# Kernel tuning notes

Measured on AMD Instinct MI355X. Metric: run time of the kernel, lower is better.

## Reference

```python
import jax, jax.numpy as jnp
import numpy as np

B, T, N, DIN, HID, ED, K = 64, 12, 1024, 2, 64, 10, 2

def setup_inputs() -> dict:
    key = jax.random.key(0)
    ks = jax.random.split(key, 18)
    g = lambda i, shape, s=0.1: jax.random.normal(ks[i], shape, jnp.float32) * s
    return dict(
        x=g(0, (B, T, N, DIN), 1.0),
        node_embeddings=g(1, (N, ED), 1.0),
        # GCRN cell 0 (dim_in=DIN): gate -> 2*HID, update -> HID
        Wg0=g(2, (ED, K, DIN + HID, 2 * HID)), bg0=g(3, (ED, 2 * HID)),
        Wu0=g(4, (ED, K, DIN + HID, HID)),     bu0=g(5, (ED, HID)),
        # GCRN cell 1 (dim_in=HID)
        Wg1=g(6, (ED, K, 2 * HID, 2 * HID)),   bg1=g(7, (ED, 2 * HID)),
        Wu1=g(8, (ED, K, 2 * HID, HID)),       bu1=g(9, (ED, HID)),
        # RelatinoShipConv: pointwise Linear(input_dim -> rnn_units), torch [out,in]
        Wr=g(10, (HID, DIN)), br=g(11, (HID,)),
        # end_conv1: Linear(HID,HID, bias=False) (num_layers>1 branch)
        W1=g(12, (HID, HID)),
        # self.conv: Conv2d(horizon, horizon, (1, HID+1), bias=False), OIHW
        Wc=g(13, (T, T, 1, HID + 1)),
        # end_conv2: Conv2d(horizon, horizon, (1, HID), bias)
        W2=g(14, (T, T, 1, HID)), b2=g(15, (T,)),
        # end_conv3: Conv2d(horizon, horizon, (1, 2), dilation (1, HID), bias)
        W3=g(16, (T, T, 1, 2)), b3=g(17, (T,)),
    )

def _avwgcn(x, supports, E, Wp, bp):
    # x:[B,N,C], supports:[K,N,N], E:[N,ED] -> [B,N,O]  (AGCRN adaptive graph conv)
    xg = jnp.einsum('knm,bmc->bnkc', supports, x)
    W = jnp.einsum('ne,ekio->nkio', E, Wp)
    b = E @ bp
    return jnp.einsum('bnki,nkio->bno', xg, W) + b

def _cell(xt, h, supports, E, Wg, bg, Wu, bu):
    # GCRN GRU cell
    zr = jax.nn.sigmoid(_avwgcn(jnp.concatenate([xt, h], -1), supports, E, Wg, bg))
    z, r = jnp.split(zr, 2, -1)
    hc = jnp.tanh(_avwgcn(jnp.concatenate([xt, z * h], -1), supports, E, Wu, bu))
    return r * h + (1.0 - r) * hc

def _conv2d(x, w, b=None, rhs_dilation=(1, 1)):
    y = jax.lax.conv_general_dilated(x, w, (1, 1), 'VALID',
        rhs_dilation=rhs_dilation, dimension_numbers=('NCHW', 'OIHW', 'NCHW'))
    return y if b is None else y + b[None, :, None, None]

def _forward(x, E, Wg0, bg0, Wu0, bu0, Wg1, bg1, Wu1, bu1, Wr, br, W1, Wc, W2, b2, W3, b3):
    A = jax.nn.softmax(jax.nn.relu(E @ E.T), axis=1)
    supports = jnp.stack([jnp.eye(N, dtype=x.dtype), A], 0)  # [K,N,N]
    # GCRN encoder: python loop over 2 layers, lax.scan over the 12 timesteps
    cur = x
    for (Wg, bg, Wu, bu) in ((Wg0, bg0, Wu0, bu0), (Wg1, bg1, Wu1, bu1)):
        h0 = jnp.zeros((x.shape[0], N, HID), x.dtype)
        def step(h, xt):
            h = _cell(xt, h, supports, E, Wg, bg, Wu, bu)
            return h, h
        _, hs = jax.lax.scan(step, h0, jnp.swapaxes(cur, 0, 1))
        cur = jnp.swapaxes(hs, 0, 1)  # [B,T,N,HID]
    out = cur @ W1.T  # end_conv1 (Linear, no bias); dropout is identity in eval
    relation = x @ Wr.T + br  # [B,T,N,HID]
    # torch einsum 'btnc,knn->kbcnt' takes the DIAGONAL of supports over n
    rg = jnp.einsum('btnc,knn->kbcnt', relation, supports)
    rg = jnp.transpose(rg, (1, 4, 3, 2, 0)).reshape(x.shape[0], T, N, -1)  # [B,12,N,2*HID]
    rst = _conv2d(rg, Wc)  # [B,12,N,HID]
    out = _conv2d(jnp.concatenate([rst, out], -1), W2, b2)  # [B,12,N,HID+1]
    out = _conv2d(out, W3, b3, rhs_dilation=(1, HID))       # [B,12,N,1]
    return out

def reference(x, node_embeddings, Wg0, bg0, Wu0, bu0, Wg1, bg1, Wu1, bu1, Wr, br, W1, Wc, W2, b2, W3, b3):
    return _forward(x, node_embeddings, Wg0, bg0, Wu0, bu0, Wg1, bg1, Wu1, bu1, Wr, br, W1, Wc, W2, b2, W3, b3)
```

## Files before the change

kernel.cpp:

```cpp
#include <hip/hip_runtime.h>

typedef unsigned short u16;
typedef unsigned int   u32;


__device__ __forceinline__ float bf2f(u16 u){ return __uint_as_float(((u32)u)<<16); }
__device__ __forceinline__ u16 f2bf(float f){
  u32 u = __float_as_uint(f);
  return (u16)((u + 0x7fffu + ((u>>16)&1u)) >> 16);
}

__global__ __launch_bounds__(256) void k_A2(const float* __restrict__ E,
    float* __restrict__ At, float* __restrict__ diagA)
{
  __shared__ float EL[10][1024];
  __shared__ float row[1024];
  __shared__ float red[4];
  int n = blockIdx.x, tid = threadIdx.x;
  for (int idx=tid; idx<10240; idx+=256)
    EL[idx>>10][idx&1023] = E[(idx&1023)*10 + (idx>>10)];
  __syncthreads();
  float en[10];
#pragma unroll
  for (int e=0;e<10;++e) en[e] = EL[e][n];
  float lmax = -1e30f;
#pragma unroll
  for (int j=0;j<4;++j){
    int m = tid*4 + j;
    float d = 0.f;
#pragma unroll
    for (int e=0;e<10;++e) d = fmaf(en[e], EL[e][m], d);
    d = fmaxf(d, 0.f);
    row[m] = d; lmax = fmaxf(lmax, d);
  }
#pragma unroll
  for (int o=32;o>0;o>>=1) lmax = fmaxf(lmax, __shfl_xor(lmax, o));
  if ((tid&63)==0) red[tid>>6] = lmax;
  __syncthreads();
  float mx = fmaxf(fmaxf(red[0],red[1]), fmaxf(red[2],red[3]));
  __syncthreads();
  float lsum = 0.f;
#pragma unroll
  for (int j=0;j<4;++j){
    int m = tid*4 + j;
    float ex = expf(row[m] - mx);
    row[m] = ex; lsum += ex;
  }
#pragma unroll
  for (int o=32;o>0;o>>=1) lsum += __shfl_xor(lsum, o);
  if ((tid&63)==0) red[tid>>6] = lsum;
  __syncthreads();
  float inv = 1.f/(red[0]+red[1]+red[2]+red[3]);
#pragma unroll
  for (int j=0;j<4;++j){
    int m = tid*4 + j;
    float v = row[m]*inv;
    At[(size_t)m*1024 + n] = v;
    if (m == n) diagA[n] = v;
  }
}

__global__ __launch_bounds__(64) void k_b3eff(
    const float* __restrict__ b2, const float* __restrict__ W3,
    const float* __restrict__ b3, float* __restrict__ b3eff)
{
  int o = threadIdx.x;
  if (o < 12){
    float a = b3[o];
    for (int i=0;i<12;++i)
      a += b2[i] * (W3[(o*12+i)*2] + W3[(o*12+i)*2+1]);
    b3eff[o] = a;
  }
}

__global__ __launch_bounds__(256) void k_Vpre(const float* __restrict__ W1,
    const float* __restrict__ W2, float* __restrict__ V)
{
  int idx = blockIdx.x*256 + threadIdx.x;
  if (idx >= 9216) return;
  int c = idx & 63, r = idx >> 6;
  int j = r % 12, i = r / 12;
  float a = 0.f;
  for (int o=0;o<64;++o)
    a = fmaf(W2[(i*12+j)*64+o], W1[o*64+c], a);
  V[idx] = a;
}

__global__ __launch_bounds__(256) void k_Gpre(const float* __restrict__ Wc,
    const float* __restrict__ W2, u16* __restrict__ G)
{
  int idx = blockIdx.x*256 + threadIdx.x;
  int u = idx & 127, r = idx >> 7;
  int ip = r % 12, i = r / 12;
  float a = 0.f;
  int wlo = u>64 ? u-64 : 0;
  int whi = u<63 ? u : 63;
  for (int j=0;j<12;++j){
    const float* w2r = W2 + (i*12+j)*64;
    const float* wcr = Wc + (j*12+ip)*65;
    for (int w=wlo; w<=whi; ++w)
      a = fmaf(w2r[w], wcr[u-w], a);
  }
  G[idx] = f2bf(a);
}

__global__ __launch_bounds__(256) void k_combF(const float* __restrict__ Wp,
    const float* __restrict__ E, float* __restrict__ out, int plane)
{
  int n = blockIdx.x;
  int j = blockIdx.y*256 + threadIdx.x;
  if (j >= plane) return;
  float a = 0.f;
#pragma unroll
  for (int e=0;e<10;++e) a = fmaf(E[n*10+e], Wp[(size_t)e*plane + j], a);
  out[(size_t)n*plane + j] = a;
}

__global__ __launch_bounds__(256) void gemm9(const float* __restrict__ At,
    const float* __restrict__ X0, float* __restrict__ Y0,
    const float* __restrict__ X1, float* __restrict__ Y1)
{
  int flat = blockIdx.x + (blockIdx.y<<3) + (blockIdx.z<<8);
  int xt = flat & 7;
  int ys = (flat>>3) & 31;
  int zs = flat >> 8;
  const float* X = zs ? X1 : X0;
  float*       Y = zs ? Y1 : Y0;
  int n0 = xt * 128;
  long baseA = (long)(2*ys) * 65536;
  long baseB = baseA + 65536;
  __shared__ float Al[2][16*128];
  __shared__ float Xl[2][16*128];
  int tid = threadIdx.x;
  int tx = tid & 15, ty = tid >> 4;
  int ka = tid >> 5,  na = (tid & 31)*4;
  int cx = tid & 31;
  long xoff = (cx < 16) ? (baseA + (long)cx*4) : (baseB + (long)(cx-16)*4);

  float accA[8][4], accB[8][4];
#pragma unroll
  for (int r=0;r<8;++r)
#pragma unroll
    for (int c=0;c<4;++c){ accA[r][c]=0.f; accB[r][c]=0.f; }

  float4 ra0 = *(const float4*)(At + (size_t)ka*1024 + n0 + na);
  float4 ra1 = *(const float4*)(At + (size_t)(ka+8)*1024 + n0 + na);
  float4 rx0 = *(const float4*)(X + xoff + (long)ka*64);
  float4 rx1 = *(const float4*)(X + xoff + (long)(ka+8)*64);

  for (int m0=0; m0<1024; m0+=16){
    int cur = (m0>>4)&1;
    *(float4*)(Al[cur] + tid*4)       = ra0;
    *(float4*)(Al[cur] + (tid+256)*4) = ra1;
    *(float4*)(Xl[cur] + tid*4)       = rx0;
    *(float4*)(Xl[cur] + (tid+256)*4) = rx1;
    __syncthreads();
    if (m0+16 < 1024){
      int m1 = m0+16;
      ra0 = *(const float4*)(At + (size_t)(m1+ka)*1024 + n0 + na);
      ra1 = *(const float4*)(At + (size_t)(m1+ka+8)*1024 + n0 + na);
      rx0 = *(const float4*)(X + xoff + (long)(m1+ka)*64);
      rx1 = *(const float4*)(X + xoff + (long)(m1+ka+8)*64);
    }
#pragma unroll
    for (int kk=0;kk<16;++kk){
      float4 a0 = *(const float4*)(Al[cur] + kk*128 + ty*4);
      float4 a1 = *(const float4*)(Al[cur] + kk*128 + 64 + ty*4);
      float4 x0 = *(const float4*)(Xl[cur] + kk*128 + tx*4);
      float4 x1 = *(const float4*)(Xl[cur] + kk*128 + 64 + tx*4);
      float av[8] = {a0.x,a0.y,a0.z,a0.w,a1.x,a1.y,a1.z,a1.w};
      float xa[4] = {x0.x,x0.y,x0.z,x0.w};
      float xb[4] = {x1.x,x1.y,x1.z,x1.w};
#pragma unroll
      for (int r=0;r<8;++r)
#pragma unroll
        for (int c=0;c<4;++c){
          accA[r][c] = fmaf(av[r], xa[c], accA[r][c]);
          accB[r][c] = fmaf(av[r], xb[c], accB[r][c]);
        }
    }
  }
#pragma unroll
  for (int r=0;r<8;++r){
    int row = n0 + (r>>2)*64 + ty*4 + (r&3);
    float4 vA; vA.x=accA[r][0]; vA.y=accA[r][1]; vA.z=accA[r][2]; vA.w=accA[r][3];
    float4 vB; vB.x=accB[r][0]; vB.y=accB[r][1]; vB.z=accB[r][2]; vB.w=accB[r][3];
    *(float4*)&Y[baseA + (long)row*64 + tx*4] = vA;
    *(float4*)&Y[baseB + (long)row*64 + tx*4] = vB;
  }
}

__global__ __launch_bounds__(256) void gemm2x(const float* __restrict__ At,
    const float* __restrict__ x, float* __restrict__ Y)
{
  __shared__ float Ats[64][65];
  __shared__ float Xs[64][65];
  int n0 = blockIdx.x*64;
  int q0 = blockIdx.y*64;
  int tid = threadIdx.x, c = tid & 63, rq = tid >> 6;
  float acc[16];
#pragma unroll
  for (int j=0;j<16;++j) acc[j]=0.f;
  for (int m0=0; m0<1024; m0+=64){
#pragma unroll
    for (int j=0;j<16;++j){
      int idx = tid + j*256;
      int k = idx>>6, r = idx&63;
      Ats[k][r] = At[(size_t)(m0+k)*1024 + n0 + r];
      int qg = q0 + r;
      Xs[k][r] = x[(size_t)(qg>>1)*2048 + (size_t)(m0+k)*2 + (qg&1)];
    }
    __syncthreads();
    for (int k=0;k<64;++k){
      float xv = Xs[k][c];
#pragma unroll
      for (int j=0;j<16;++j) acc[j] = fmaf(Ats[k][rq+4*j], xv, acc[j]);
    }
    __syncthreads();
  }
#pragma unroll
  for (int j=0;j<16;++j)
    Y[(size_t)(n0+rq+4*j)*1536 + q0 + c] = acc[j];
}

template<int L>
__device__ __forceinline__ void gate_body(
    float* __restrict__ inp, float* __restrict__ Wl, float* __restrict__ En,
    const float* __restrict__ Wg, const float* __restrict__ Wpre,
    const float* __restrict__ bgp, const float* __restrict__ E,
    const float* __restrict__ xsrc, const float* __restrict__ Axt,
    const float* __restrict__ h, const float* __restrict__ Ah,
    float* __restrict__ zh, float* __restrict__ rb, int t, int first,
    int n, int b0, int tid)
{
  constexpr int IX  = (L==0)?2:64;
  constexpr int KI  = 2*(IX+64);
  constexpr int CH  = (L==0)?44:32;
  constexpr int NCH = KI/CH;
  constexpr int O   = 128;

  if (tid < 10) En[tid] = E[n*10 + tid];
  for (int idx=tid; idx<32*IX; idx+=256){
    int bl = idx/IX, i = idx - bl*IX; int b = b0+bl;
    inp[bl*KI + i] = (L==0)
      ? xsrc[(size_t)((b*12+t)*1024+n)*2 + i]
      : xsrc[((size_t)b<<16) + (size_t)n*64 + i];
  }
  for (int idx=tid; idx<2048; idx+=256){
    int bl = idx>>6, c = idx&63; int b = b0+bl;
    inp[bl*KI + IX + c] = first ? 0.f : h[((size_t)b<<16) + (size_t)n*64 + c];
  }
  for (int idx=tid; idx<32*IX; idx+=256){
    int bl = idx/IX, i = idx - bl*IX; int b = b0+bl;
    inp[bl*KI + IX+64+i] = (L==0)
      ? Axt[(size_t)n*1536 + (size_t)(b*12+t)*2 + i]
      : Axt[((size_t)b<<16) + (size_t)n*64 + i];
  }
  for (int idx=tid; idx<2048; idx+=256){
    int bl = idx>>6, c = idx&63; int b = b0+bl;
    inp[bl*KI + 2*IX+64+c] = first ? 0.f : Ah[((size_t)b<<16) + (size_t)n*64 + c];
  }
  __syncthreads();

  int bg = tid >> 5;
  int og = tid & 31;
  float acc[4][4];
#pragma unroll
  for (int d=0;d<4;++d){
    int o = og*4+d;
    float a = 0.f;
#pragma unroll
    for (int e=0;e<10;++e) a = fmaf(En[e], bgp[e*O+o], a);
#pragma unroll
    for (int bl=0;bl<4;++bl) acc[bl][d] = a;
  }

  for (int ch=0; ch<NCH; ++ch){
    if (Wpre){
      const float* src = Wpre + (size_t)n*(KI*O) + ch*CH*O;
      for (int idx=tid; idx<CH*O; idx+=256) Wl[idx] = src[idx];
    } else {
      for (int idx=tid; idx<CH*O; idx+=256){
        int i = idx>>7, o = idx&127;
        float a = 0.f;
#pragma unroll
        for (int e=0;e<10;++e)
          a = fmaf(En[e], Wg[((size_t)e*KI + ch*CH + i)*O + o], a);
        Wl[i*O + o] = a;
      }
    }
    __syncthreads();
    float4 xq[4], wq[4];
#pragma unroll
    for (int bl=0;bl<4;++bl) xq[bl] = *(const float4*)&inp[(bg*4+bl)*KI + ch*CH];
#pragma unroll
    for (int ii=0;ii<4;++ii) wq[ii] = *(const float4*)&Wl[ii*O + og*4];
    for (int i=0; i<CH; i+=4){
      int i2 = (i+4<CH) ? i+4 : i;
      float4 xq2[4], wq2[4];
#pragma unroll
      for (int bl=0;bl<4;++bl) xq2[bl] = *(const float4*)&inp[(bg*4+bl)*KI + ch*CH + i2];
#pragma unroll
      for (int ii=0;ii<4;++ii) wq2[ii] = *(const float4*)&Wl[(i2+ii)*O + og*4];
      float xv[4][4], wv[4][4];
#pragma unroll
      for (int bl=0;bl<4;++bl){ xv[bl][0]=xq[bl].x; xv[bl][1]=xq[bl].y; xv[bl][2]=xq[bl].z; xv[bl][3]=xq[bl].w; }
#pragma unroll
      for (int ii=0;ii<4;++ii){ wv[ii][0]=wq[ii].x; wv[ii][1]=wq[ii].y; wv[ii][2]=wq[ii].z; wv[ii][3]=wq[ii].w; }
#pragma unroll
      for (int bl=0;bl<4;++bl)
#pragma unroll
        for (int d=0;d<4;++d)
#pragma unroll
          for (int ii=0;ii<4;++ii)
            acc[bl][d] = fmaf(xv[bl][ii], wv[ii][d], acc[bl][d]);
#pragma unroll
      for (int bl=0;bl<4;++bl) xq[bl]=xq2[bl];
#pragma unroll
      for (int ii=0;ii<4;++ii) wq[ii]=wq2[ii];
    }
    __syncthreads();
  }

#pragma unroll
  for (int bl=0;bl<4;++bl){
    int b = b0 + bg*4 + bl;
    size_t base = ((size_t)b<<16) + (size_t)n*64;
#pragma unroll
    for (int d=0;d<4;++d){
      int o = og*4 + d;
      float s = 1.f/(1.f+__expf(-acc[bl][d]));
      if (o < 64){
        if (!first) zh[base+o] = s * h[base+o];
      } else {
        rb[base+o-64] = s;
      }
    }
  }
}

__global__ __launch_bounds__(256) void k_gateB(int l_z0,
    const float* __restrict__ Wg0, const float* __restrict__ Wg0p,
    const float* __restrict__ bg0,
    const float* __restrict__ Wg1, const float* __restrict__ Wg1p,
    const float* __restrict__ bg1,
    const float* __restrict__ E,  const float* __restrict__ x,
    const float* __restrict__ Ax0T,
    const float* __restrict__ h0cur, const float* __restrict__ h1,
    const float* __restrict__ Axt1,  const float* __restrict__ AhZ1,
    float* __restrict__ zh0, float* __restrict__ rb0,
    float* __restrict__ zh1, float* __restrict__ rb1,
    int t0, int first0, int first1)
{
  __shared__ float smem[12288];
  __shared__ float En[10];
  int n = blockIdx.x, b0 = blockIdx.y*32, tid = threadIdx.x;
  int L = blockIdx.z ? 0 : l_z0;
  if (L == 1)
    gate_body<1>(smem, smem + 32*256, En, Wg1, Wg1p, bg1, E,
                 h0cur, Axt1, h1, AhZ1, zh1, rb1, 0, first1, n, b0, tid);
  else
    gate_body<0>(smem, smem + 32*132, En, Wg0, Wg0p, bg0, E,
                 x, Ax0T, h0cur, Axt1, zh0, rb0, t0, first0, n, b0, tid);
}

template<int L>
__device__ __forceinline__ void upd_body(
    float* __restrict__ inp, float* __restrict__ Wl, float* __restrict__ En,
    const float* __restrict__ Wu, const float* __restrict__ Wpre,
    const float* __restrict__ bup, const float* __restrict__ E,
    const float* __restrict__ xsrc, const float* __restrict__ Axt,
    const float* __restrict__ zh, const float* __restrict__ Azh,
    const float* __restrict__ rb,
    const float* __restrict__ hread, float* __restrict__ hwrite,
    const float* __restrict__ V, float* __restrict__ q1acc,
    int t, int tq, int first, int n, int b0, int tid)
{
  constexpr int IX  = (L==0)?2:64;
  constexpr int KI  = 2*(IX+64);
  constexpr int CH  = (L==0)?44:64;
  constexpr int NCH = KI/CH;
  constexpr int O   = 64;

  if (tid < 10) En[tid] = E[n*10 + tid];
  for (int idx=tid; idx<32*IX; idx+=256){
    int bl = idx/IX, i = idx - bl*IX; int b = b0+bl;
    inp[bl*KI + i] = (L==0)
      ? xsrc[(size_t)((b*12+t)*1024+n)*2 + i]
      : xsrc[((size_t)b<<16) + (size_t)n*64 + i];
  }
  for (int idx=tid; idx<2048; idx+=256){
    int bl = idx>>6, c = idx&63; int b = b0+bl;
    inp[bl*KI + IX + c] = first ? 0.f : zh[((size_t)b<<16) + (size_t)n*64 + c];
  }
  for (int idx=tid; idx<32*IX; idx+=256){
    int bl = idx/IX, i = idx - bl*IX; int b = b0+bl;
    inp[bl*KI + IX+64+i] = (L==0)
      ? Axt[(size_t)n*1536 + (size_t)(b*12+t)*2 + i]
      : Axt[((size_t)b<<16) + (size_t)n*64 + i];
  }
  for (int idx=tid; idx<2048; idx+=256){
    int bl = idx>>6, c = idx&63; int b = b0+bl;
    inp[bl*KI + 2*IX+64+c] = first ? 0.f : Azh[((size_t)b<<16) + (size_t)n*64 + c];
  }
  __syncthreads();

  int bg = tid >> 5;
  int og = tid & 31;
  float acc[4][2];
#pragma unroll
  for (int d=0;d<2;++d){
    int o = og*2+d;
    float a = 0.f;
#pragma unroll
    for (int e=0;e<10;++e) a = fmaf(En[e], bup[e*O+o], a);
#pragma unroll
    for (int bl=0;bl<4;++bl) acc[bl][d] = a;
  }

  for (int ch=0; ch<NCH; ++ch){
    if (Wpre){
      const float* src = Wpre + (size_t)n*(KI*O) + ch*CH*O;
      for (int idx=tid; idx<CH*O; idx+=256) Wl[idx] = src[idx];
    } else {
      for (int idx=tid; idx<CH*O; idx+=256){
        int i = idx>>6, o = idx&63;
        float a = 0.f;
#pragma unroll
        for (int e=0;e<10;++e)
          a = fmaf(En[e], Wu[((size_t)e*KI + ch*CH + i)*O + o], a);
        Wl[i*O + o] = a;
      }
    }
    __syncthreads();
    float4 xq[4]; float2 wq[4];
#pragma unroll
    for (int bl=0;bl<4;++bl) xq[bl] = *(const float4*)&inp[(bg*4+bl)*KI + ch*CH];
#pragma unroll
    for (int ii=0;ii<4;++ii) wq[ii] = *(const float2*)&Wl[ii*O + og*2];
    for (int i=0; i<CH; i+=4){
      int i2 = (i+4<CH) ? i+4 : i;
      float4 xq2[4]; float2 wq2[4];
#pragma unroll
      for (int bl=0;bl<4;++bl) xq2[bl] = *(const float4*)&inp[(bg*4+bl)*KI + ch*CH + i2];
#pragma unroll
      for (int ii=0;ii<4;++ii) wq2[ii] = *(const float2*)&Wl[(i2+ii)*O + og*2];
      float xv[4][4], wv[4][2];
#pragma unroll
      for (int bl=0;bl<4;++bl){ xv[bl][0]=xq[bl].x; xv[bl][1]=xq[bl].y; xv[bl][2]=xq[bl].z; xv[bl][3]=xq[bl].w; }
#pragma unroll
      for (int ii=0;ii<4;++ii){ wv[ii][0]=wq[ii].x; wv[ii][1]=wq[ii].y; }
#pragma unroll
      for (int bl=0;bl<4;++bl)
#pragma unroll
        for (int d=0;d<2;++d)
#pragma unroll
          for (int ii=0;ii<4;++ii)
            acc[bl][d] = fmaf(xv[bl][ii], wv[ii][d], acc[bl][d]);
#pragma unroll
      for (int bl=0;bl<4;++bl) xq[bl]=xq2[bl];
#pragma unroll
      for (int ii=0;ii<4;++ii) wq[ii]=wq2[ii];
    }
    __syncthreads();
  }

  float* hnL = Wl;
  float* VL  = Wl + 2080;
#pragma unroll
  for (int bl=0;bl<4;++bl){
    int b = b0 + bg*4 + bl;
    size_t base = ((size_t)b<<16) + (size_t)n*64;
#pragma unroll
    for (int d=0;d<2;++d){
      int o = og*2 + d;
      float hc = tanhf(acc[bl][d]);
      float r  = rb[base+o];
      float h0v = first ? 0.f : hread[base+o];
      float hn = r*h0v + (1.f-r)*hc;
      hwrite[base+o] = hn;
      if (L==1) hnL[(bg*4+bl)*65 + o] = hn;
    }
  }
  if (L==1){
    for (int idx=tid; idx<768; idx+=256)
      VL[idx] = V[((idx>>6)*12+tq)*64 + (idx&63)];
    __syncthreads();
    for (int task=tid; task<384; task+=256){
      int bl = task & 31, i = task >> 5;
      const float* hv = hnL + bl*65;
      const float* vv = VL + i*64;
      float s = 0.f;
#pragma unroll 8
      for (int c=0;c<64;++c) s = fmaf(hv[c], vv[c], s);
      size_t qi = (((size_t)(b0+bl)<<10) + n)*12 + i;
      if (first) q1acc[qi] = s; else q1acc[qi] += s;
    }
  }
}

__global__ __launch_bounds__(256) void k_updB(int l_z0,
    const float* __restrict__ Wu0, const float* __restrict__ Wu0p,
    const float* __restrict__ bu0,
    const float* __restrict__ Wu1, const float* __restrict__ Wu1p,
    const float* __restrict__ bu1,
    const float* __restrict__ E,  const float* __restrict__ x,
    const float* __restrict__ Ax0T, const float* __restrict__ Axt1,
    const float* __restrict__ h0cur, float* __restrict__ h0new,
    float* __restrict__ h1,
    const float* __restrict__ zh0, const float* __restrict__ Azh0,
    const float* __restrict__ rb0,
    const float* __restrict__ zh1, const float* __restrict__ Azh1,
    const float* __restrict__ rb1,
    const float* __restrict__ V, float* __restrict__ q1acc,
    int t0, int t1, int first0, int first1)
{
  __shared__ float smem[12288];
  __shared__ float En[10];
  int n = blockIdx.x, b0 = blockIdx.y*32, tid = threadIdx.x;
  int L = blockIdx.z ? 0 : l_z0;
  if (L == 1)
    upd_body<1>(smem, smem + 32*256, En, Wu1, Wu1p, bu1, E,
                h0cur, Axt1, zh1, Azh1, rb1, h1, h1, V, q1acc,
                0, t1, first1, n, b0, tid);
  else
    upd_body<0>(smem, smem + 32*132, En, Wu0, Wu0p, bu0, E,
                x, Ax0T, zh0, Azh0, rb0, h0cur, h0new, nullptr, nullptr,
                t0, 0, first0, n, b0, tid);
}

__global__ __launch_bounds__(256) void k_q0G(
    const float* __restrict__ x, const float* __restrict__ diagA,
    const u16* __restrict__ G,
    const float* __restrict__ Wr, const float* __restrict__ br,
    float* __restrict__ q0buf)
{
  int n = blockIdx.x, tid = threadIdx.x;
  __shared__ u16  GL[18432];
  __shared__ float xsL[64][25];
  __shared__ float WrL[64][2];
  __shared__ float brL[64];

  for (int idx=tid; idx<18432; idx+=256) GL[idx] = G[idx];
  for (int idx=tid; idx<1536; idx+=256){
    int b = idx/24, r = idx - b*24;
    xsL[b][r] = x[(size_t)((b*12+(r>>1))*1024+n)*2 + (r&1)];
  }
  if (tid<128) WrL[tid>>1][tid&1] = Wr[tid];
  else if (tid<192) brL[tid-128] = br[tid-128];
  __syncthreads();

  float dA = diagA[n];
  int b = tid & 63, iq = tid >> 6;
  int i0 = iq*3;
  float q0a=0.f, q0b=0.f, q0c=0.f;
  for (int ip=0; ip<12; ++ip){
    float xa = xsL[b][ip*2], xb = xsL[b][ip*2+1];
    const u16* g0r = &GL[((i0+0)*12+ip)*128];
    const u16* g1r = &GL[((i0+1)*12+ip)*128];
    const u16* g2r = &GL[((i0+2)*12+ip)*128];
    for (int c=0;c<64;++c){
      float rel  = fmaf(xa, WrL[c][0], fmaf(xb, WrL[c][1], brL[c]));
      float relD = rel * dA;
      u32 g0 = *(const u32*)&g0r[2*c];
      u32 g1 = *(const u32*)&g1r[2*c];
      u32 g2 = *(const u32*)&g2r[2*c];
      q0a = fmaf(rel, bf2f((u16)g0), fmaf(relD, bf2f((u16)(g0>>16)), q0a));
      q0b = fmaf(rel, bf2f((u16)g1), fmaf(relD, bf2f((u16)(g1>>16)), q0b));
      q0c = fmaf(rel, bf2f((u16)g2), fmaf(relD, bf2f((u16)(g2>>16)), q0c));
    }
  }
  size_t qb = (((size_t)b<<10) + n)*12;
  q0buf[qb+i0]   = q0a;
  q0buf[qb+i0+1] = q0b;
  q0buf[qb+i0+2] = q0c;
}

__global__ __launch_bounds__(256) void k_head2(
    const float* __restrict__ q0buf, const float* __restrict__ q1acc,
    const float* __restrict__ W3, const float* __restrict__ b3eff,
    float* __restrict__ out)
{
  int n = blockIdx.x, tid = threadIdx.x;
  __shared__ float W3L[12][12][2];
  __shared__ float b3eL[12];
  __shared__ float q0L[64][12];
  __shared__ float q1L[64][12];

  if (tid < 12) b3eL[tid] = b3eff[tid];
  for (int idx=tid; idx<288; idx+=256){
    int o = idx/24, r = idx - o*24;
    W3L[o][r>>1][r&1] = W3[idx];
  }
  for (int idx=tid; idx<768; idx+=256){
    int b = idx/12, i = idx - (idx/12)*12;
    size_t base = (((size_t)b<<10) + n)*12 + i;
    q0L[b][i] = q0buf[base];
    q1L[b][i] = q1acc[base];
  }
  __syncthreads();

  for (int idx=tid; idx<768; idx+=256){
    int bb = idx/12, o = idx - (idx/12)*12;
    float a = b3eL[o];
#pragma unroll
    for (int i=0;i<12;++i)
      a += q0L[bb][i]*W3L[o][i][0] + q1L[bb][i]*W3L[o][i][1];
    out[(size_t)(bb*12+o)*1024 + n] = a;
  }
}

extern "C" void kernel_launch(void* const* d_in, const int* in_sizes, int n_in,
                              void* d_out, int out_size, void* d_ws, size_t ws_size,
                              hipStream_t stream)
{
  const float* x   = (const float*)d_in[0];
  const float* E   = (const float*)d_in[1];
  const float* Wg0 = (const float*)d_in[2];
  const float* bg0 = (const float*)d_in[3];
  const float* Wu0 = (const float*)d_in[4];
  const float* bu0 = (const float*)d_in[5];
  const float* Wg1 = (const float*)d_in[6];
  const float* bg1 = (const float*)d_in[7];
  const float* Wu1 = (const float*)d_in[8];
  const float* bu1 = (const float*)d_in[9];
  const float* Wr  = (const float*)d_in[10];
  const float* br  = (const float*)d_in[11];
  const float* W1  = (const float*)d_in[12];
  const float* Wc  = (const float*)d_in[13];
  const float* W2  = (const float*)d_in[14];
  const float* b2  = (const float*)d_in[15];
  const float* W3  = (const float*)d_in[16];
  const float* b3  = (const float*)d_in[17];

  char* ws = (char*)d_ws;
  size_t off = 0;
  auto alloc = [&](size_t bytes)->void*{
    void* p = ws + off; off += (bytes + 255) & ~(size_t)255; return p;
  };
  float* At    = (float*)alloc(1024ull*1024*4);
  float* diagA = (float*)alloc(1024*4);
  float* Ax0T  = (float*)alloc(1024ull*1536*4);
  float* Axt1  = (float*)alloc(64ull*65536*4);
  float* AhZ1  = (float*)alloc(64ull*65536*4);
  float* Azh0  = (float*)alloc(64ull*65536*4);
  float* Azh1  = (float*)alloc(64ull*65536*4);
  float* zh0   = (float*)alloc(64ull*65536*4);
  float* zh1   = (float*)alloc(64ull*65536*4);
  float* rb0   = (float*)alloc(64ull*65536*4);
  float* rb1   = (float*)alloc(64ull*65536*4);
  float* h0a   = (float*)alloc(64ull*65536*4);
  float* h0b   = (float*)alloc(64ull*65536*4);
  float* h1    = (float*)alloc(64ull*65536*4);
  float* q1acc = (float*)alloc(64ull*1024*12*4);
  float* q0buf = (float*)alloc(64ull*1024*12*4);
  float* V     = (float*)alloc(12ull*12*64*4);
  u16*   G     = (u16*)alloc(12ull*12*128*2);
  float* b3eff = (float*)alloc(12*4);

  if (off > ws_size) return;

  auto tryAlloc = [&](size_t bytes)->float*{
    size_t aligned = (bytes + 255) & ~(size_t)255;
    if (off + aligned > ws_size) return (float*)nullptr;
    void* p = ws + off; off += aligned; return (float*)p;
  };
  float* Wg1c = tryAlloc(1024ull*32768*4);
  float* Wu1c = tryAlloc(1024ull*16384*4);
  float* Wg0c = tryAlloc(1024ull*16896*4);
  float* Wu0c = tryAlloc(1024ull*8448*4);

  k_A2<<<dim3(1024),256,0,stream>>>(E, At, diagA);
  k_b3eff<<<dim3(1),64,0,stream>>>(b2, W3, b3, b3eff);
  k_Vpre<<<dim3(36),256,0,stream>>>(W1, W2, V);
  k_Gpre<<<dim3(72),256,0,stream>>>(Wc, W2, G);
  if (Wg1c) k_combF<<<dim3(1024,128),256,0,stream>>>(Wg1, E, Wg1c, 32768);
  if (Wu1c) k_combF<<<dim3(1024, 64),256,0,stream>>>(Wu1, E, Wu1c, 16384);
  if (Wg0c) k_combF<<<dim3(1024, 66),256,0,stream>>>(Wg0, E, Wg0c, 16896);
  if (Wu0c) k_combF<<<dim3(1024, 33),256,0,stream>>>(Wu0, E, Wu0c,  8448);
  gemm2x<<<dim3(16,24),256,0,stream>>>(At, x, Ax0T);
  k_q0G<<<dim3(1024),256,0,stream>>>(x, diagA, G, Wr, br, q0buf);

  k_gateB<<<dim3(1024,2,1),256,0,stream>>>(0, Wg0,Wg0c,bg0, Wg1,Wg1c,bg1,
      E, x, Ax0T, h0a, h1, Axt1, AhZ1, zh0, rb0, zh1, rb1, 0, 1, 0);
  k_updB<<<dim3(1024,2,1),256,0,stream>>>(0, Wu0,Wu0c,bu0, Wu1,Wu1c,bu1,
      E, x, Ax0T, Axt1, h0a, h0a, h1, zh0, Azh0, rb0, zh1, Azh1, rb1,
      V, q1acc, 0, 0, 1, 0);
  gemm9<<<dim3(8,32,1),256,0,stream>>>(At, h0a, Axt1, nullptr, nullptr);

  for (int k=0; k<12; ++k){
    int last   = (k == 11);
    int first1 = (k == 0);
    float* h0cur = (k&1) ? h0b : h0a;
    float* h0new = (k&1) ? h0a : h0b;

    k_gateB<<<dim3(1024,2, last?1:2),256,0,stream>>>(1, Wg0,Wg0c,bg0,
        Wg1,Wg1c,bg1, E, x, Ax0T, h0cur, h1, Axt1, AhZ1,
        zh0, rb0, zh1, rb1, k+1, 0, first1);

    if (first1)
      gemm9<<<dim3(8,32,1),256,0,stream>>>(At, zh0, Azh0, nullptr, nullptr);
    else if (last)
      gemm9<<<dim3(8,32,1),256,0,stream>>>(At, zh1, Azh1, nullptr, nullptr);
    else
      gemm9<<<dim3(8,32,2),256,0,stream>>>(At, zh1, Azh1, zh0, Azh0);

    k_updB<<<dim3(1024,2, last?1:2),256,0,stream>>>(1, Wu0,Wu0c,bu0,
        Wu1,Wu1c,bu1, E, x, Ax0T, Axt1, h0cur, h0new, h1,
        zh0, Azh0, rb0, zh1, Azh1, rb1, V, q1acc, k+1, k, 0, first1);

    if (!last)
      gemm9<<<dim3(8,32,2),256,0,stream>>>(At, h1, AhZ1, h0new, Axt1);
  }

  k_head2<<<dim3(1024),256,0,stream>>>(q0buf, q1acc, W3, b3eff, (float*)d_out);
}
```

Baseline: 9.957 ms.

## Process all 64 batches per node block to halve per-node weight loads

```diff
diff --git a/kernel.cpp b/kernel.cpp
--- a/kernel.cpp
+++ b/kernel.cpp
@@ -225,54 +225,53 @@
 
 template<int L>
 __device__ __forceinline__ void gate_body(
-    float* __restrict__ inp, float* __restrict__ Wl, float* __restrict__ En,
+    float* __restrict__ inp, float* __restrict__ Wl,
     const float* __restrict__ Wg, const float* __restrict__ Wpre,
     const float* __restrict__ bgp, const float* __restrict__ E,
     const float* __restrict__ xsrc, const float* __restrict__ Axt,
     const float* __restrict__ h, const float* __restrict__ Ah,
     float* __restrict__ zh, float* __restrict__ rb, int t, int first,
-    int n, int b0, int tid)
+    int n, int tid)
 {
   constexpr int IX  = (L==0)?2:64;
   constexpr int KI  = 2*(IX+64);
-  constexpr int CH  = (L==0)?44:32;
+  constexpr int CH  = (L==0)?44:16;
   constexpr int NCH = KI/CH;
   constexpr int O   = 128;
 
-  if (tid < 10) En[tid] = E[n*10 + tid];
-  for (int idx=tid; idx<32*IX; idx+=256){
-    int bl = idx/IX, i = idx - bl*IX; int b = b0+bl;
+  for (int idx=tid; idx<64*IX; idx+=256){
+    int bl = idx/IX, i = idx - bl*IX;
     inp[bl*KI + i] = (L==0)
-      ? xsrc[(size_t)((b*12+t)*1024+n)*2 + i]
-      : xsrc[((size_t)b<<16) + (size_t)n*64 + i];
-  }
-  for (int idx=tid; idx<2048; idx+=256){
-    int bl = idx>>6, c = idx&63; int b = b0+bl;
-    inp[bl*KI + IX + c] = first ? 0.f : h[((size_t)b<<16) + (size_t)n*64 + c];
-  }
-  for (int idx=tid; idx<32*IX; idx+=256){
-    int bl = idx/IX, i = idx - bl*IX; int b = b0+bl;
+      ? xsrc[(size_t)((bl*12+t)*1024+n)*2 + i]
+      : xsrc[((size_t)bl<<16) + (size_t)n*64 + i];
+  }
+  for (int idx=tid; idx<4096; idx+=256){
+    int bl = idx>>6, c = idx&63;
+    inp[bl*KI + IX + c] = first ? 0.f : h[((size_t)bl<<16) + (size_t)n*64 + c];
+  }
+  for (int idx=tid; idx<64*IX; idx+=256){
+    int bl = idx/IX, i = idx - bl*IX;
     inp[bl*KI + IX+64+i] = (L==0)
-      ? Axt[(size_t)n*1536 + (size_t)(b*12+t)*2 + i]
-      : Axt[((size_t)b<<16) + (size_t)n*64 + i];
-  }
-  for (int idx=tid; idx<2048; idx+=256){
-    int bl = idx>>6, c = idx&63; int b = b0+bl;
-    inp[bl*KI + 2*IX+64+c] = first ? 0.f : Ah[((size_t)b<<16) + (size_t)n*64 + c];
+      ? Axt[(size_t)n*1536 + (size_t)(bl*12+t)*2 + i]
+      : Axt[((size_t)bl<<16) + (size_t)n*64 + i];
+  }
+  for (int idx=tid; idx<4096; idx+=256){
+    int bl = idx>>6, c = idx&63;
+    inp[bl*KI + 2*IX+64+c] = first ? 0.f : Ah[((size_t)bl<<16) + (size_t)n*64 + c];
   }
   __syncthreads();
 
   int bg = tid >> 5;
   int og = tid & 31;
-  float acc[4][4];
+  float acc[8][4];
 #pragma unroll
   for (int d=0;d<4;++d){
     int o = og*4+d;
     float a = 0.f;
 #pragma unroll
-    for (int e=0;e<10;++e) a = fmaf(En[e], bgp[e*O+o], a);
-#pragma unroll
-    for (int bl=0;bl<4;++bl) acc[bl][d] = a;
+    for (int e=0;e<10;++e) a = fmaf(E[n*10+e], bgp[e*O+o], a);
+#pragma unroll
+    for (int bb=0;bb<8;++bb) acc[bb][d] = a;
   }
 
   for (int ch=0; ch<NCH; ++ch){
@@ -285,51 +284,41 @@
         float a = 0.f;
 #pragma unroll
         for (int e=0;e<10;++e)
-          a = fmaf(En[e], Wg[((size_t)e*KI + ch*CH + i)*O + o], a);
+          a = fmaf(E[n*10+e], Wg[((size_t)e*KI + ch*CH + i)*O + o], a);
         Wl[i*O + o] = a;
       }
     }
     __syncthreads();
-    float4 xq[4], wq[4];
-#pragma unroll
-    for (int bl=0;bl<4;++bl) xq[bl] = *(const float4*)&inp[(bg*4+bl)*KI + ch*CH];
-#pragma unroll
-    for (int ii=0;ii<4;++ii) wq[ii] = *(const float4*)&Wl[ii*O + og*4];
     for (int i=0; i<CH; i+=4){
-      int i2 = (i+4<CH) ? i+4 : i;
-      float4 xq2[4], wq2[4];
-#pragma unroll
-      for (int bl=0;bl<4;++bl) xq2[bl] = *(const float4*)&inp[(bg*4+bl)*KI + ch*CH + i2];
-#pragma unroll
-      for (int ii=0;ii<4;++ii) wq2[ii] = *(const float4*)&Wl[(i2+ii)*O + og*4];
-      float xv[4][4], wv[4][4];
-#pragma unroll
-      for (int bl=0;bl<4;++bl){ xv[bl][0]=xq[bl].x; xv[bl][1]=xq[bl].y; xv[bl][2]=xq[bl].z; xv[bl][3]=xq[bl].w; }
+      float4 xq[8], wq[4];
+#pragma unroll
+      for (int bb=0;bb<8;++bb) xq[bb] = *(const float4*)&inp[(bg*8+bb)*KI + ch*CH + i];
+#pragma unroll
+      for (int ii=0;ii<4;++ii) wq[ii] = *(const float4*)&Wl[(i+ii)*O + og*4];
+      float xv[8][4], wv[4][4];
+#pragma unroll
+      for (int bb=0;bb<8;++bb){ xv[bb][0]=xq[bb].x; xv[bb][1]=xq[bb].y; xv[bb][2]=xq[bb].z; xv[bb][3]=xq[bb].w; }
 #pragma unroll
       for (int ii=0;ii<4;++ii){ wv[ii][0]=wq[ii].x; wv[ii][1]=wq[ii].y; wv[ii][2]=wq[ii].z; wv[ii][3]=wq[ii].w; }
 #pragma unroll
-      for (int bl=0;bl<4;++bl)
+      for (int bb=0;bb<8;++bb)
 #pragma unroll
         for (int d=0;d<4;++d)
 #pragma unroll
           for (int ii=0;ii<4;++ii)
-            acc[bl][d] = fmaf(xv[bl][ii], wv[ii][d], acc[bl][d]);
-#pragma unroll
-      for (int bl=0;bl<4;++bl) xq[bl]=xq2[bl];
-#pragma unroll
-      for (int ii=0;ii<4;++ii) wq[ii]=wq2[ii];
-    }
-    __syncthreads();
-  }
-
-#pragma unroll
-  for (int bl=0;bl<4;++bl){
-    int b = b0 + bg*4 + bl;
+            acc[bb][d] = fmaf(xv[bb][ii], wv[ii][d], acc[bb][d]);
+    }
+    __syncthreads();
+  }
+
+#pragma unroll
+  for (int bb=0;bb<8;++bb){
+    int b = bg*8 + bb;
     size_t base = ((size_t)b<<16) + (size_t)n*64;
 #pragma unroll
     for (int d=0;d<4;++d){
       int o = og*4 + d;
-      float s = 1.f/(1.f+__expf(-acc[bl][d]));
+      float s = 1.f/(1.f+__expf(-acc[bb][d]));
       if (o < 64){
         if (!first) zh[base+o] = s * h[base+o];
       } else {
@@ -339,7 +328,7 @@
   }
 }
 
-__global__ __launch_bounds__(256) void k_gateB(int l_z0,
+__global__ __launch_bounds__(256) void k_gateB(int l_y0,
     const float* __restrict__ Wg0, const float* __restrict__ Wg0p,
     const float* __restrict__ bg0,
     const float* __restrict__ Wg1, const float* __restrict__ Wg1p,
@@ -352,21 +341,20 @@
     float* __restrict__ zh1, float* __restrict__ rb1,
     int t0, int first0, int first1)
 {
-  __shared__ float smem[12288];
-  __shared__ float En[10];
-  int n = blockIdx.x, b0 = blockIdx.y*32, tid = threadIdx.x;
-  int L = blockIdx.z ? 0 : l_z0;
+  __shared__ float smem[18432];
+  int n = blockIdx.x, tid = threadIdx.x;
+  int L = blockIdx.y ? 0 : l_y0;
   if (L == 1)
-    gate_body<1>(smem, smem + 32*256, En, Wg1, Wg1p, bg1, E,
-                 h0cur, Axt1, h1, AhZ1, zh1, rb1, 0, first1, n, b0, tid);
+    gate_body<1>(smem, smem + 64*256, Wg1, Wg1p, bg1, E,
+                 h0cur, Axt1, h1, AhZ1, zh1, rb1, 0, first1, n, tid);
   else
-    gate_body<0>(smem, smem + 32*132, En, Wg0, Wg0p, bg0, E,
-                 x, Ax0T, h0cur, Axt1, zh0, rb0, t0, first0, n, b0, tid);
+    gate_body<0>(smem, smem + 64*132, Wg0, Wg0p, bg0, E,
+                 x, Ax0T, h0cur, Axt1, zh0, rb0, t0, first0, n, tid);
 }
 
 template<int L>
 __device__ __forceinline__ void upd_body(
-    float* __restrict__ inp, float* __restrict__ Wl, float* __restrict__ En,
+    float* __restrict__ inp, float* __restrict__ Wl,
     const float* __restrict__ Wu, const float* __restrict__ Wpre,
     const float* __restrict__ bup, const float* __restrict__ E,
     const float* __restrict__ xsrc, const float* __restrict__ Axt,
@@ -374,48 +362,47 @@
     const float* __restrict__ rb,
     const float* __restrict__ hread, float* __restrict__ hwrite,
     const float* __restrict__ V, float* __restrict__ q1acc,
-    int t, int tq, int first, int n, int b0, int tid)
+    int t, int tq, int first, int n, int tid)
 {
   constexpr int IX  = (L==0)?2:64;
   constexpr int KI  = 2*(IX+64);
-  constexpr int CH  = (L==0)?44:64;
+  constexpr int CH  = (L==0)?44:32;
   constexpr int NCH = KI/CH;
   constexpr int O   = 64;
 
-  if (tid < 10) En[tid] = E[n*10 + tid];
-  for (int idx=tid; idx<32*IX; idx+=256){
-    int bl = idx/IX, i = idx - bl*IX; int b = b0+bl;
+  for (int idx=tid; idx<64*IX; idx+=256){
+    int bl = idx/IX, i = idx - bl*IX;
     inp[bl*KI + i] = (L==0)
-      ? xsrc[(size_t)((b*12+t)*1024+n)*2 + i]
-      : xsrc[((size_t)b<<16) + (size_t)n*64 + i];
-  }
-  for (int idx=tid; idx<2048; idx+=256){
-    int bl = idx>>6, c = idx&63; int b = b0+bl;
-    inp[bl*KI + IX + c] = first ? 0.f : zh[((size_t)b<<16) + (size_t)n*64 + c];
-  }
-  for (int idx=tid; idx<32*IX; idx+=256){
-    int bl = idx/IX, i = idx - bl*IX; int b = b0+bl;
+      ? xsrc[(size_t)((bl*12+t)*1024+n)*2 + i]
+      : xsrc[((size_t)bl<<16) + (size_t)n*64 + i];
+  }
+  for (int idx=tid; idx<4096; idx+=256){
+    int bl = idx>>6, c = idx&63;
+    inp[bl*KI + IX + c] = first ? 0.f : zh[((size_t)bl<<16) + (size_t)n*64 + c];
+  }
+  for (int idx=tid; idx<64*IX; idx+=256){
+    int bl = idx/IX, i = idx - bl*IX;
     inp[bl*KI + IX+64+i] = (L==0)
-      ? Axt[(size_t)n*1536 + (size_t)(b*12+t)*2 + i]
-      : Axt[((size_t)b<<16) + (size_t)n*64 + i];
-  }
-  for (int idx=tid; idx<2048; idx+=256){
-    int bl = idx>>6, c = idx&63; int b = b0+bl;
-    inp[bl*KI + 2*IX+64+c] = first ? 0.f : Azh[((size_t)b<<16) + (size_t)n*64 + c];
+      ? Axt[(size_t)n*1536 + (size_t)(bl*12+t)*2 + i]
+      : Axt[((size_t)bl<<16) + (size_t)n*64 + i];
+  }
+  for (int idx=tid; idx<4096; idx+=256){
+    int bl = idx>>6, c = idx&63;
+    inp[bl*KI + 2*IX+64+c] = first ? 0.f : Azh[((size_t)bl<<16) + (size_t)n*64 + c];
   }
   __syncthreads();
 
   int bg = tid >> 5;
   int og = tid & 31;
-  float acc[4][2];
+  float acc[8][2];
 #pragma unroll
   for (int d=0;d<2;++d){
     int o = og*2+d;
     float a = 0.f;
 #pragma unroll
-    for (int e=0;e<10;++e) a = fmaf(En[e], bup[e*O+o], a);
-#pragma unroll
-    for (int bl=0;bl<4;++bl) acc[bl][d] = a;
+    for (int e=0;e<10;++e) a = fmaf(E[n*10+e], bup[e*O+o], a);
+#pragma unroll
+    for (int bb=0;bb<8;++bb) acc[bb][d] = a;
   }
 
   for (int ch=0; ch<NCH; ++ch){
@@ -428,78 +415,68 @@
         float a = 0.f;
 #pragma unroll
         for (int e=0;e<10;++e)
-          a = fmaf(En[e], Wu[((size_t)e*KI + ch*CH + i)*O + o], a);
+          a = fmaf(E[n*10+e], Wu[((size_t)e*KI + ch*CH + i)*O + o], a);
         Wl[i*O + o] = a;
       }
     }
     __syncthreads();
-    float4 xq[4]; float2 wq[4];
-#pragma unroll
-    for (int bl=0;bl<4;++bl) xq[bl] = *(const float4*)&inp[(bg*4+bl)*KI + ch*CH];
-#pragma unroll
-    for (int ii=0;ii<4;++ii) wq[ii] = *(const float2*)&Wl[ii*O + og*2];
     for (int i=0; i<CH; i+=4){
-      int i2 = (i+4<CH) ? i+4 : i;
-      float4 xq2[4]; float2 wq2[4];
-#pragma unroll
-      for (int bl=0;bl<4;++bl) xq2[bl] = *(const float4*)&inp[(bg*4+bl)*KI + ch*CH + i2];
-#pragma unroll
-      for (int ii=0;ii<4;++ii) wq2[ii] = *(const float2*)&Wl[(i2+ii)*O + og*2];
-      float xv[4][4], wv[4][2];
-#pragma unroll
-      for (int bl=0;bl<4;++bl){ xv[bl][0]=xq[bl].x; xv[bl][1]=xq[bl].y; xv[bl][2]=xq[bl].z; xv[bl][3]=xq[bl].w; }
+      float4 xq[8]; float2 wq[4];
+#pragma unroll
+      for (int bb=0;bb<8;++bb) xq[bb] = *(const float4*)&inp[(bg*8+bb)*KI + ch*CH + i];
+#pragma unroll
+      for (int ii=0;ii<4;++ii) wq[ii] = *(const float2*)&Wl[(i+ii)*O + og*2];
+      float xv[8][4], wv[4][2];
+#pragma unroll
+      for (int bb=0;bb<8;++bb){ xv[bb][0]=xq[bb].x; xv[bb][1]=xq[bb].y; xv[bb][2]=xq[bb].z; xv[bb][3]=xq[bb].w; }
 #pragma unroll
       for (int ii=0;ii<4;++ii){ wv[ii][0]=wq[ii].x; wv[ii][1]=wq[ii].y; }
 #pragma unroll
-      for (int bl=0;bl<4;++bl)
+      for (int bb=0;bb<8;++bb)
 #pragma unroll
         for (int d=0;d<2;++d)
 #pragma unroll
           for (int ii=0;ii<4;++ii)
-            acc[bl][d] = fmaf(xv[bl][ii], wv[ii][d], acc[bl][d]);
-#pragma unroll
-      for (int bl=0;bl<4;++bl) xq[bl]=xq2[bl];
-#pragma unroll
-      for (int ii=0;ii<4;++ii) wq[ii]=wq2[ii];
-    }
-    __syncthreads();
-  }
-
-  float* hnL = Wl;
-  float* VL  = Wl + 2080;
-#pragma unroll
-  for (int bl=0;bl<4;++bl){
-    int b = b0 + bg*4 + bl;
+            acc[bb][d] = fmaf(xv[bb][ii], wv[ii][d], acc[bb][d]);
+    }
+    __syncthreads();
+  }
+
+  float* hnL = inp;
+  float* VL  = inp + 4160;
+#pragma unroll
+  for (int bb=0;bb<8;++bb){
+    int b = bg*8 + bb;
     size_t base = ((size_t)b<<16) + (size_t)n*64;
 #pragma unroll
     for (int d=0;d<2;++d){
       int o = og*2 + d;
-      float hc = tanhf(acc[bl][d]);
+      float hc = tanhf(acc[bb][d]);
       float r  = rb[base+o];
       float h0v = first ? 0.f : hread[base+o];
       float hn = r*h0v + (1.f-r)*hc;
       hwrite[base+o] = hn;
-      if (L==1) hnL[(bg*4+bl)*65 + o] = hn;
+      if (L==1) hnL[b*65 + o] = hn;
     }
   }
   if (L==1){
     for (int idx=tid; idx<768; idx+=256)
       VL[idx] = V[((idx>>6)*12+tq)*64 + (idx&63)];
     __syncthreads();
-    for (int task=tid; task<384; task+=256){
-      int bl = task & 31, i = task >> 5;
+    for (int task=tid; task<768; task+=256){
+      int bl = task & 63, i = task >> 6;
       const float* hv = hnL + bl*65;
       const float* vv = VL + i*64;
       float s = 0.f;
 #pragma unroll 8
       for (int c=0;c<64;++c) s = fmaf(hv[c], vv[c], s);
-      size_t qi = (((size_t)(b0+bl)<<10) + n)*12 + i;
+      size_t qi = (((size_t)bl<<10) + n)*12 + i;
       if (first) q1acc[qi] = s; else q1acc[qi] += s;
     }
   }
 }
 
-__global__ __launch_bounds__(256) void k_updB(int l_z0,
+__global__ __launch_bounds__(256) void k_updB(int l_y0,
     const float* __restrict__ Wu0, const float* __restrict__ Wu0p,
     const float* __restrict__ bu0,
     const float* __restrict__ Wu1, const float* __restrict__ Wu1p,
@@ -515,18 +492,17 @@
     const float* __restrict__ V, float* __restrict__ q1acc,
     int t0, int t1, int first0, int first1)
 {
-  __shared__ float smem[12288];
-  __shared__ float En[10];
-  int n = blockIdx.x, b0 = blockIdx.y*32, tid = threadIdx.x;
-  int L = blockIdx.z ? 0 : l_z0;
+  __shared__ float smem[18432];
+  int n = blockIdx.x, tid = threadIdx.x;
+  int L = blockIdx.y ? 0 : l_y0;
   if (L == 1)
-    upd_body<1>(smem, smem + 32*256, En, Wu1, Wu1p, bu1, E,
+    upd_body<1>(smem, smem + 64*256, Wu1, Wu1p, bu1, E,
                 h0cur, Axt1, zh1, Azh1, rb1, h1, h1, V, q1acc,
-                0, t1, first1, n, b0, tid);
+                0, t1, first1, n, tid);
   else
-    upd_body<0>(smem, smem + 32*132, En, Wu0, Wu0p, bu0, E,
+    upd_body<0>(smem, smem + 64*132, Wu0, Wu0p, bu0, E,
                 x, Ax0T, zh0, Azh0, rb0, h0cur, h0new, nullptr, nullptr,
-                t0, 0, first0, n, b0, tid);
+                t0, 0, first0, n, tid);
 }
 
 __global__ __launch_bounds__(256) void k_q0G(
@@ -665,25 +641,25 @@
     if (off + aligned > ws_size) return (float*)nullptr;
     void* p = ws + off; off += aligned; return (float*)p;
   };
-  float* Wg1c = tryAlloc(1024ull*32768*4);
+  float* Wu0c = tryAlloc(1024ull*8448*4);
   float* Wu1c = tryAlloc(1024ull*16384*4);
   float* Wg0c = tryAlloc(1024ull*16896*4);
-  float* Wu0c = tryAlloc(1024ull*8448*4);
+  float* Wg1c = tryAlloc(1024ull*32768*4);
 
   k_A2<<<dim3(1024),256,0,stream>>>(E, At, diagA);
   k_b3eff<<<dim3(1),64,0,stream>>>(b2, W3, b3, b3eff);
   k_Vpre<<<dim3(36),256,0,stream>>>(W1, W2, V);
   k_Gpre<<<dim3(72),256,0,stream>>>(Wc, W2, G);
-  if (Wg1c) k_combF<<<dim3(1024,128),256,0,stream>>>(Wg1, E, Wg1c, 32768);
+  if (Wu0c) k_combF<<<dim3(1024, 33),256,0,stream>>>(Wu0, E, Wu0c,  8448);
   if (Wu1c) k_combF<<<dim3(1024, 64),256,0,stream>>>(Wu1, E, Wu1c, 16384);
   if (Wg0c) k_combF<<<dim3(1024, 66),256,0,stream>>>(Wg0, E, Wg0c, 16896);
-  if (Wu0c) k_combF<<<dim3(1024, 33),256,0,stream>>>(Wu0, E, Wu0c,  8448);
+  if (Wg1c) k_combF<<<dim3(1024,128),256,0,stream>>>(Wg1, E, Wg1c, 32768);
   gemm2x<<<dim3(16,24),256,0,stream>>>(At, x, Ax0T);
   k_q0G<<<dim3(1024),256,0,stream>>>(x, diagA, G, Wr, br, q0buf);
 
-  k_gateB<<<dim3(1024,2,1),256,0,stream>>>(0, Wg0,Wg0c,bg0, Wg1,Wg1c,bg1,
+  k_gateB<<<dim3(1024,1),256,0,stream>>>(0, Wg0,Wg0c,bg0, Wg1,Wg1c,bg1,
       E, x, Ax0T, h0a, h1, Axt1, AhZ1, zh0, rb0, zh1, rb1, 0, 1, 0);
-  k_updB<<<dim3(1024,2,1),256,0,stream>>>(0, Wu0,Wu0c,bu0, Wu1,Wu1c,bu1,
+  k_updB<<<dim3(1024,1),256,0,stream>>>(0, Wu0,Wu0c,bu0, Wu1,Wu1c,bu1,
       E, x, Ax0T, Axt1, h0a, h0a, h1, zh0, Azh0, rb0, zh1, Azh1, rb1,
       V, q1acc, 0, 0, 1, 0);
   gemm9<<<dim3(8,32,1),256,0,stream>>>(At, h0a, Axt1, nullptr, nullptr);
@@ -694,7 +670,7 @@
     float* h0cur = (k&1) ? h0b : h0a;
     float* h0new = (k&1) ? h0a : h0b;
 
-    k_gateB<<<dim3(1024,2, last?1:2),256,0,stream>>>(1, Wg0,Wg0c,bg0,
+    k_gateB<<<dim3(1024, last?1:2),256,0,stream>>>(1, Wg0,Wg0c,bg0,
         Wg1,Wg1c,bg1, E, x, Ax0T, h0cur, h1, Axt1, AhZ1,
         zh0, rb0, zh1, rb1, k+1, 0, first1);
 
@@ -705,7 +681,7 @@
     else
       gemm9<<<dim3(8,32,2),256,0,stream>>>(At, zh1, Azh1, zh0, Azh0);
 
-    k_updB<<<dim3(1024,2, last?1:2),256,0,stream>>>(1, Wu0,Wu0c,bu0,
+    k_updB<<<dim3(1024, last?1:2),256,0,stream>>>(1, Wu0,Wu0c,bu0,
         Wu1,Wu1c,bu1, E, x, Ax0T, Axt1, h0cur, h0new, h1,
         zh0, Azh0, rb0, zh1, Azh1, rb1, V, q1acc, k+1, k, 0, first1);
 
```

Measured after the change: 11.97 ms. 1.2x slower.
